# Performance work log

Hardware: AMD Instinct MI355X
Metric: run time of the kernel (lower is better)

Reference implementation:

```python
import jax, jax.numpy as jnp
import numpy as np

NQ = 4  # n_qubits_per_head


def _apply_ry(state, theta, q):
    # state: (N, 2,2,2,2) real amplitudes; theta: (N,) per-element angle; wire q
    st = jnp.moveaxis(state, 1 + q, -1)
    c = jnp.cos(0.5 * theta).reshape(-1, 1, 1, 1)
    s = jnp.sin(0.5 * theta).reshape(-1, 1, 1, 1)
    a0, a1 = st[..., 0], st[..., 1]
    st = jnp.stack([c * a0 - s * a1, s * a0 + c * a1], axis=-1)
    return jnp.moveaxis(st, -1, 1 + q)


def _apply_cnot(state, ctrl, tgt):
    st = jnp.moveaxis(state, (1 + ctrl, 1 + tgt), (-2, -1))
    st = jnp.stack([st[..., 0, :], st[..., 1, ::-1]], axis=-2)
    return jnp.moveaxis(st, (-2, -1), (1 + ctrl, 1 + tgt))


def _quantum_circuit(x_in, par):
    # x_in: (N, NQ) data angles; par: (N, L, NQ) variational angles (per head, tiled)
    N = x_in.shape[0]
    L = par.shape[1]
    state = jnp.zeros((N, 2, 2, 2, 2), x_in.dtype).at[:, 0, 0, 0, 0].set(1.0)
    for l in range(L):
        for q in range(NQ):
            state = _apply_ry(state, par[:, l, q], q)
        for q in range(NQ - 1):
            state = _apply_cnot(state, q, q + 1)
        state = _apply_cnot(state, NQ - 1, 0)
    for q in range(NQ):
        state = _apply_ry(state, x_in[:, q], q)
    p = state * state  # probabilities (real amplitudes: only RY/CNOT gates)
    zs = []
    for q in range(NQ):
        st = jnp.moveaxis(p, 1 + q, -1)
        zs.append(jnp.sum(st[..., 0], axis=(1, 2, 3)) - jnp.sum(st[..., 1], axis=(1, 2, 3)))
    return jnp.stack(zs, axis=-1)  # (N, NQ)


def setup_inputs() -> dict:
    key = jax.random.key(0)
    ks = jax.random.split(key, 6)
    B, T, E, H, L = 4, 2048, 1024, 16, 2
    scale = 1.0 / np.sqrt(E)
    x = jax.random.normal(ks[0], (B, T, E), dtype=jnp.float32)
    Wq = jax.random.normal(ks[1], (E, E), dtype=jnp.float32) * scale
    Wk = jax.random.normal(ks[2], (E, E), dtype=jnp.float32) * scale
    Wv = jax.random.normal(ks[3], (E, E), dtype=jnp.float32) * scale
    Wo = jax.random.normal(ks[4], (E, E), dtype=jnp.float32) * scale
    qparams = jax.random.normal(ks[5], (H, L, NQ), dtype=jnp.float32)
    return {"x": x, "Wq": Wq, "Wk": Wk, "Wv": Wv, "Wo": Wo, "qparams": qparams}


def reference(x, Wq, Wk, Wv, Wo, qparams):
    B, T, E = x.shape
    H, L, _ = qparams.shape
    hd = E // H
    q = x @ Wq.T
    k = x @ Wk.T
    v = x @ Wv.T
    # NOTE: original scales by sqrt(embed_dim), not sqrt(head_dim)
    scores = jnp.einsum('bte,bse->bts', q, k) / jnp.sqrt(jnp.asarray(E, x.dtype))
    w = jax.nn.softmax(scores, axis=-1)
    out = jnp.einsum('bts,bse->bte', w, v)
    oh = out.reshape(B, T, H, hd)
    N = B * T * H
    xin = oh[..., :NQ].reshape(N, NQ)
    par = jnp.broadcast_to(qparams[None, None], (B, T, H, L, NQ)).reshape(N, L, NQ)
    z = _quantum_circuit(xin, par)  # (N, NQ)
    zfull = jnp.concatenate([z, jnp.zeros((N, hd - NQ), x.dtype)], axis=-1)
    return zfull.reshape(B, T, E) @ Wo.T
```

## Files before the change

### kernel.cpp

```cpp
#include <hip/hip_runtime.h>
#include <hip/hip_fp16.h>

typedef _Float16 half_t;
typedef __attribute__((ext_vector_type(8))) _Float16 half8;
typedef __attribute__((ext_vector_type(4))) float floatx4;

__device__ __forceinline__ void async_copy16(const void* src, void* dst_lds) {
  __builtin_amdgcn_global_load_lds(
      (__attribute__((address_space(1))) void*)src,
      (__attribute__((address_space(3))) void*)dst_lds, 16, 0, 0);
}

__global__ __launch_bounds__(512, 2) void gemm_nt_256(
    const half_t* __restrict__ A, const half_t* __restrict__ B,
    half_t* __restrict__ C,
    int lda, int ldb, int ldc, int kIters,
    long sAz2, long sBz2, long sCz2, float scale)
{
  __shared__ __align__(16) half_t sm[2][2][256 * 64];

  const int tid  = threadIdx.x;
  const int wave = tid >> 6, lane = tid & 63;
  const int wm = wave >> 2, wn = wave & 3;
  const int er = lane >> 4, ec = lane & 15;
  const int sw = ec & 7;

  const long z = blockIdx.z;
  const half_t* Ab = A + (long)blockIdx.x * 256 * lda + z * sAz2;
  const half_t* Bb = B + (long)blockIdx.y * 256 * ldb + z * sBz2;

  const int srow = tid >> 3;
  const int skq  = (tid & 7) ^ (srow & 7);

  floatx4 acc[2][2][4][2];
  #pragma unroll
  for (int a = 0; a < 2; a++)
    #pragma unroll
    for (int b = 0; b < 2; b++)
      #pragma unroll
      for (int i = 0; i < 4; i++)
        #pragma unroll
        for (int j = 0; j < 2; j++)
          acc[a][b][i][j] = (floatx4){0.f, 0.f, 0.f, 0.f};

#define STAGE_A(bb, hf, kt) do {                                              \
    const half_t* Ak_ = Ab + (long)(kt) * 64;                                 \
    _Pragma("unroll")                                                         \
    for (int r_ = 0; r_ < 2; r_++) {                                          \
      int lrow_ = r_ * 64 + srow;                                             \
      async_copy16(Ak_ + (long)((hf) * 128 + lrow_) * lda + skq * 8,          \
                   &sm[(bb)][0][(hf) * 8192 + (r_ * 512 + wave * 64) * 8]);   \
    } } while (0)

#define STAGE_B(bb, hf, kt) do {                                              \
    const half_t* Bk_ = Bb + (long)(kt) * 64;                                 \
    _Pragma("unroll")                                                         \
    for (int r_ = 0; r_ < 2; r_++) {                                          \
      int lrow_ = r_ * 64 + srow;                                             \
      async_copy16(Bk_ + (long)((hf) * 128 + lrow_) * ldb + skq * 8,          \
                   &sm[(bb)][1][(hf) * 8192 + (r_ * 512 + wave * 64) * 8]);   \
    } } while (0)

#define DS_A(DST, BB, MH, KS) do {                                            \
    _Pragma("unroll")                                                         \
    for (int ii = 0; ii < 4; ii++) {                                          \
      int row_ = (MH) * 128 + wm * 64 + ii * 16 + ec;                         \
      DST[ii] = *(const half8*)                                               \
          &sm[BB][0][row_ * 64 + ((((KS) * 4 + er) ^ sw) * 8)];               \
    } } while (0)

#define DS_B(DST, BB, KS) do {                                                \
    _Pragma("unroll")                                                         \
    for (int nj = 0; nj < 4; nj++) {                                          \
      int row_ = (nj >> 1) * 128 + wn * 32 + (nj & 1) * 16 + ec;              \
      DST[nj] = *(const half8*)                                               \
          &sm[BB][1][row_ * 64 + ((((KS) * 4 + er) ^ sw) * 8)];               \
    } } while (0)

#define MFMA16(AF, BF, MH) do {                                               \
    __builtin_amdgcn_s_setprio(1);                                            \
    _Pragma("unroll")                                                         \
    for (int ii = 0; ii < 4; ii++)                                            \
      _Pragma("unroll")                                                       \
      for (int nj = 0; nj < 4; nj++)                                          \
        acc[MH][nj >> 1][ii][nj & 1] =                                        \
            __builtin_amdgcn_mfma_f32_16x16x32_f16(                           \
                AF[ii], BF[nj], acc[MH][nj >> 1][ii][nj & 1], 0, 0, 0);       \
    __builtin_amdgcn_s_setprio(0);                                            \
  } while (0)

#define BAR() __builtin_amdgcn_s_barrier()
#define VMW(N) asm volatile("s_waitcnt vmcnt(" #N ")" ::: "memory")

  half8 afA[4], afB[4], bfA[4], bfB[4];
  int cur = 0;
  const int nt = kIters;

  STAGE_B(0, 0, 0); STAGE_B(0, 1, 0); STAGE_A(0, 0, 0); STAGE_A(0, 1, 0);
  VMW(2);
  BAR();
  DS_A(afA, 0, 0, 0);
  DS_B(bfA, 0, 0);

  for (int n = 0; n < nt; ++n) {
    const int hasNext = (n + 1 < nt);
    DS_A(afB, cur, 0, 1);
    DS_B(bfB, cur, 1);
    if (hasNext) { STAGE_B(cur ^ 1, 0, n + 1); STAGE_B(cur ^ 1, 1, n + 1); }
    MFMA16(afA, bfA, 0);
    if (hasNext) { VMW(4); } else { VMW(0); }
    BAR();
    DS_A(afA, cur, 1, 0);
    if (hasNext) STAGE_A(cur ^ 1, 0, n + 1);
    MFMA16(afB, bfB, 0);
    BAR();
    DS_A(afB, cur, 1, 1);
    if (hasNext) STAGE_A(cur ^ 1, 1, n + 1);
    MFMA16(afA, bfA, 1);
    if (hasNext) VMW(2);
    BAR();
    if (hasNext) {
      DS_A(afA, cur ^ 1, 0, 0);
      DS_B(bfA, cur ^ 1, 0);
    }
    MFMA16(afB, bfB, 1);
    BAR();
    cur ^= 1;
  }

#undef STAGE_A
#undef STAGE_B
#undef DS_A
#undef DS_B
#undef MFMA16
#undef BAR
#undef VMW

  const long rowBase = (long)blockIdx.x * 256;
  const long colBase = (long)blockIdx.y * 256;
  half_t* Cz = C + z * sCz2;
  #pragma unroll
  for (int mh = 0; mh < 2; mh++)
    #pragma unroll
    for (int nh = 0; nh < 2; nh++)
      #pragma unroll
      for (int ii = 0; ii < 4; ii++)
        #pragma unroll
        for (int jj = 0; jj < 2; jj++)
          #pragma unroll
          for (int r = 0; r < 4; r++) {
            long row = rowBase + mh * 128 + wm * 64 + ii * 16 + er * 4 + r;
            long col = colBase + nh * 128 + wn * 32 + jj * 16 + ec;
            Cz[row * (long)ldc + col] =
                (_Float16)(acc[mh][nh][ii][jj][r] * scale);
          }
}

template<int BN, int EPI>
__global__ __launch_bounds__(256) void gemm_nt(
    const half_t* __restrict__ A, const half_t* __restrict__ B,
    void* __restrict__ Cout,
    int lda, int ldb, int ldc, int kIters, int zShift,
    long sAz1, long sBz1, long sCz1,
    long sAz2, long sBz2, long sCz2, float scale,
    const float* __restrict__ qab)
{
  constexpr int BM = 128;
  constexpr int WN = BN / 2;
  constexpr int AN = WN / 16;
  constexpr int RA = BM * 8 / 256;
  constexpr int RB = BN * 8 / 256;
  __shared__ __align__(16) half_t lA[BM * 64];
  __shared__ __align__(16) half_t lB[BN * 64];

  const int tid  = threadIdx.x;
  const int wave = tid >> 6, lane = tid & 63;
  const int wm = wave >> 1, wn = wave & 1;
  const int er = lane >> 4, ec = lane & 15;
  const int sw = ec & 7;

  const long z = blockIdx.z;
  const long z2 = z >> zShift;
  const long z1 = z - (z2 << zShift);
  const half_t* Ab = A + (long)blockIdx.x * BM * lda + z1 * sAz1 + z2 * sAz2;
  const half_t* Bb = B + (long)blockIdx.y * BN * ldb + z1 * sBz1 + z2 * sBz2;
  const long cz = z1 * sCz1 + z2 * sCz2;

  floatx4 acc[4][AN];
  #pragma unroll
  for (int i = 0; i < 4; i++)
    #pragma unroll
    for (int j = 0; j < AN; j++)
      acc[i][j] = (floatx4){0.f, 0.f, 0.f, 0.f};

  for (int ks = 0; ks < kIters; ++ks) {
    const half_t* Ak = Ab + ks * 64;
    const half_t* Bk = Bb + ks * 64;
    #pragma unroll
    for (int r = 0; r < RA; r++) {
      int s = r * 256 + tid;
      int row = s >> 3;
      int kq = (s & 7) ^ (row & 7);
      async_copy16(Ak + (long)row * lda + kq * 8,
                   &lA[(r * 256 + wave * 64) * 8]);
    }
    #pragma unroll
    for (int r = 0; r < RB; r++) {
      int s = r * 256 + tid;
      int row = s >> 3;
      int kq = (s & 7) ^ (row & 7);
      async_copy16(Bk + (long)row * ldb + kq * 8,
                   &lB[(r * 256 + wave * 64) * 8]);
    }
    __syncthreads();

    #pragma unroll
    for (int h = 0; h < 2; h++) {
      half8 af[4], bfv[AN];
      #pragma unroll
      for (int i = 0; i < 4; i++) {
        int row = wm * 64 + i * 16 + ec;
        af[i] = *(const half8*)&lA[row * 64 + (((h * 4 + er) ^ sw) * 8)];
      }
      #pragma unroll
      for (int j = 0; j < AN; j++) {
        int row = wn * WN + j * 16 + ec;
        bfv[j] = *(const half8*)&lB[row * 64 + (((h * 4 + er) ^ sw) * 8)];
      }
      #pragma unroll
      for (int i = 0; i < 4; i++)
        #pragma unroll
        for (int j = 0; j < AN; j++)
          acc[i][j] = __builtin_amdgcn_mfma_f32_16x16x32_f16(
              af[i], bfv[j], acc[i][j], 0, 0, 0);
    }
    __syncthreads();
  }

  const long rowBase = (long)blockIdx.x * BM + wm * 64;
  const long colBase = (long)blockIdx.y * BN + wn * WN;
  #pragma unroll
  for (int i = 0; i < 4; i++)
    #pragma unroll
    for (int j = 0; j < AN; j++)
      #pragma unroll
      for (int r = 0; r < 4; r++) {
        long row = rowBase + i * 16 + er * 4 + r;
        long col = colBase + j * 16 + ec;
        float v = acc[i][j][r];
        if constexpr (EPI == 0) {
          ((half_t*)Cout)[cz + row * (long)ldc + col] = (_Float16)(v * scale);
        } else if constexpr (EPI == 1) {
          ((half_t*)Cout)[cz + col * (long)ldc + row] = (_Float16)v;
        } else if constexpr (EPI == 2) {
          ((float*)Cout)[cz + row * (long)ldc + col] = v * scale;
        } else {
          float za = qab[2 * (int)col], zb = qab[2 * (int)col + 1];
          float zv = za * cosf(v) + zb * sinf(v);
          ((half_t*)Cout)[cz + row * (long)ldc + col] = (_Float16)zv;
        }
      }
}

__global__ __launch_bounds__(256) void softmax_rows(half_t* __restrict__ S,
                                                    int ld)
{
  const long row = blockIdx.x;
  half8* sp = (half8*)(S + row * (long)ld);
  const int t = threadIdx.x;
  const int wave = t >> 6, lane = t & 63;
  half8 hv = sp[t];
  float e[8];
  #pragma unroll
  for (int k = 0; k < 8; k++) e[k] = (float)hv[k];
  float m = e[0];
  #pragma unroll
  for (int k = 1; k < 8; k++) m = fmaxf(m, e[k]);
  #pragma unroll
  for (int o = 32; o > 0; o >>= 1) m = fmaxf(m, __shfl_xor(m, o));
  __shared__ float rmax[4], rsum[4];
  if (lane == 0) rmax[wave] = m;
  __syncthreads();
  m = fmaxf(fmaxf(rmax[0], rmax[1]), fmaxf(rmax[2], rmax[3]));
  float s = 0.f;
  #pragma unroll
  for (int k = 0; k < 8; k++) { e[k] = expf(e[k] - m); s += e[k]; }
  #pragma unroll
  for (int o = 32; o > 0; o >>= 1) s += __shfl_xor(s, o);
  if (lane == 0) rsum[wave] = s;
  __syncthreads();
  float inv = 1.f / (rsum[0] + rsum[1] + rsum[2] + rsum[3]);
  half8 o8;
  #pragma unroll
  for (int k = 0; k < 8; k++) o8[k] = (_Float16)(e[k] * inv);
  sp[t] = o8;
}

__global__ __launch_bounds__(256) void prep_all(
    const float* __restrict__ x,  const float* __restrict__ Wq,
    const float* __restrict__ Wk, const float* __restrict__ Wv,
    const float* __restrict__ Wo, const float* __restrict__ qp, int L,
    half_t* __restrict__ xh, half_t* __restrict__ Wqk,
    half_t* __restrict__ Wv4, half_t* __restrict__ Wos,
    float* __restrict__ qab)
{
  const int bid = blockIdx.x;
  if (bid < 4096) {
    long i = ((long)bid * 256 + threadIdx.x) * 8;
    float4 a = *(const float4*)(x + i);
    float4 b = *(const float4*)(x + i + 4);
    half8 h = {(_Float16)a.x, (_Float16)a.y, (_Float16)a.z, (_Float16)a.w,
               (_Float16)b.x, (_Float16)b.y, (_Float16)b.z, (_Float16)b.w};
    *(half8*)(xh + i) = h;
  } else if (bid < 5120) {
    long i = ((long)(bid - 4096) * 256 + threadIdx.x) * 8;
    int r = (int)(i >> 10);
    int e = (int)(i & 1023);
    const float* src = (r < 1024 ? Wq + (long)r * 1024
                                 : Wk + (long)(r - 1024) * 1024) + e;
    float4 a = *(const float4*)src;
    float4 b = *(const float4*)(src + 4);
    half8 h = {(_Float16)a.x, (_Float16)a.y, (_Float16)a.z, (_Float16)a.w,
               (_Float16)b.x, (_Float16)b.y, (_Float16)b.z, (_Float16)b.w};
    *(half8*)(Wqk + i) = h;
  } else if (bid < 5152) {
    long i = ((long)(bid - 5120) * 256 + threadIdx.x) * 8;
    int c = (int)(i >> 10);
    int e = (int)(i & 1023);
    const float* src = Wv + (long)(((c >> 2) << 6) | (c & 3)) * 1024 + e;
    float4 a = *(const float4*)src;
    float4 b = *(const float4*)(src + 4);
    half8 h = {(_Float16)a.x, (_Float16)a.y, (_Float16)a.z, (_Float16)a.w,
               (_Float16)b.x, (_Float16)b.y, (_Float16)b.z, (_Float16)b.w};
    *(half8*)(Wv4 + i) = h;
  } else if (bid < 5408) {
    int idx = (bid - 5152) * 256 + threadIdx.x;
    int e = idx >> 6, c = idx & 63;
    Wos[idx] = (_Float16)Wo[(long)e * 1024 + (((c >> 2) << 6) | (c & 3))];
  } else {
    int h = threadIdx.x;
    if (h >= 16) return;
    float st[16];
    #pragma unroll
    for (int i = 0; i < 16; i++) st[i] = 0.f;
    st[0] = 1.f;
    for (int l = 0; l < L; l++) {
      #pragma unroll
      for (int q = 0; q < 4; q++) {
        float th = qp[(h * L + l) * 4 + q];
        float c = cosf(0.5f * th), s = sinf(0.5f * th);
        int mq = 8 >> q;
        #pragma unroll
        for (int i = 0; i < 16; i++) {
          if ((i & mq) == 0) {
            float a0 = st[i], a1 = st[i | mq];
            st[i]      = c * a0 - s * a1;
            st[i | mq] = s * a0 + c * a1;
          }
        }
      }
      const int cm[4] = {8, 4, 2, 1};
      const int tm[4] = {4, 2, 1, 8};
      #pragma unroll
      for (int p = 0; p < 4; p++) {
        int mc = cm[p], mt = tm[p];
        #pragma unroll
        for (int i = 0; i < 16; i++) {
          if ((i & mc) != 0 && (i & mt) == 0) {
            float tv = st[i]; st[i] = st[i | mt]; st[i | mt] = tv;
          }
        }
      }
    }
    #pragma unroll
    for (int q = 0; q < 4; q++) {
      int mq = 8 >> q;
      float zc = 0.f, xc = 0.f;
      #pragma unroll
      for (int i = 0; i < 16; i++) {
        float p2 = st[i] * st[i];
        zc += ((i & mq) == 0) ? p2 : -p2;
        if ((i & mq) == 0) xc += st[i] * st[i | mq];
      }
      qab[(h * 4 + q) * 2 + 0] = zc;
      qab[(h * 4 + q) * 2 + 1] = -2.f * xc;
    }
  }
}

extern "C" void kernel_launch(void* const* d_in, const int* in_sizes, int n_in,
                              void* d_out, int out_size, void* d_ws, size_t ws_size,
                              hipStream_t stream)
{
  const float* x  = (const float*)d_in[0];
  const float* Wq = (const float*)d_in[1];
  const float* Wk = (const float*)d_in[2];
  const float* Wv = (const float*)d_in[3];
  const float* Wo = (const float*)d_in[4];
  const float* qp = (const float*)d_in[5];
  const int L = in_sizes[5] / 64;
  float* out = (float*)d_out;

  char* w = (char*)d_ws;
  size_t off = 0;
  auto alloc = [&](size_t bytes) -> void* {
    void* p = w + off;
    off = (off + bytes + 255) & ~(size_t)255;
    return p;
  };
  float*  qab  = (float*)alloc(512);
  half_t* xh   = (half_t*)alloc((size_t)8192 * 1024 * 2);
  half_t* Wqk  = (half_t*)alloc((size_t)2048 * 1024 * 2);
  half_t* Wv4  = (half_t*)alloc((size_t)64 * 1024 * 2);
  half_t* Wos  = (half_t*)alloc((size_t)1024 * 64 * 2);
  half_t* V4th = (half_t*)alloc((size_t)64 * 8192 * 2);
  half_t* Z4   = (half_t*)alloc((size_t)8192 * 64 * 2);

  half_t* QKb = (half_t*)d_out;

  int tier = (ws_size >= off + (size_t)8192 * 2048 * 2 + 256) ? 0 : 1;
  const size_t Sn = (tier == 0) ? (size_t)8192 * 2048 : (size_t)2048 * 2048;
  half_t* S = (half_t*)alloc(Sn * 2);

  prep_all<<<dim3(5409), dim3(256), 0, stream>>>(
      x, Wq, Wk, Wv, Wo, qp, L, xh, Wqk, Wv4, Wos, qab);

  gemm_nt_256<<<dim3(32, 8, 1), 512, 0, stream>>>(
      xh, Wqk, QKb, 1024, 1024, 2048, 16, 0, 0, 0, 1.f);
  gemm_nt<64, 1><<<dim3(64, 1, 1), 256, 0, stream>>>(
      xh, Wv4, V4th, 1024, 1024, 8192, 16, 0,
      0, 0, 0, 0, 0, 0, 1.f, nullptr);

  if (tier == 0) {
    gemm_nt_256<<<dim3(8, 8, 4), 512, 0, stream>>>(
        QKb, QKb + 1024, S, 2048, 2048, 2048, 16,
        (long)2048 * 2048, (long)2048 * 2048, (long)2048 * 2048, 0.03125f);
    softmax_rows<<<dim3(8192), dim3(256), 0, stream>>>(S, 2048);
    gemm_nt<64, 5><<<dim3(16, 1, 4), 256, 0, stream>>>(
        S, V4th, Z4, 2048, 8192, 64, 32, 0,
        0, 0, 0, (long)2048 * 2048, 2048, (long)2048 * 64, 1.f, qab);
  } else {
    for (int b = 0; b < 4; b++) {
      const long q0 = (long)b * 2048;
      gemm_nt<128, 0><<<dim3(16, 16, 1), 256, 0, stream>>>(
          QKb + q0 * 2048, QKb + 1024 + q0 * 2048, S,
          2048, 2048, 2048, 16, 0, 0, 0, 0, 0, 0, 0, 0.03125f, nullptr);
      softmax_rows<<<dim3(2048), dim3(256), 0, stream>>>(S, 2048);
      gemm_nt<64, 5><<<dim3(16, 1, 1), 256, 0, stream>>>(
          S, V4th + q0, Z4 + q0 * 64, 2048, 8192, 64, 32, 0,
          0, 0, 0, 0, 0, 0, 1.f, qab);
    }
  }

  gemm_nt<128, 2><<<dim3(64, 8, 1), 256, 0, stream>>>(
      Z4, Wos, out, 64, 64, 1024, 1, 0,
      0, 0, 0, 0, 0, 0, 1.f, nullptr);
}
```

Before: 239.7 us.

## Split-K the V and PV skinny GEMMs with separate reduction kernels

The skinny V4 projection GEMM (64 blocks) and the attention-times-V GEMM (64 blocks) each underfill the GPU. They are now split along K into 4 fp32 partial outputs, giving 256 blocks per launch, and small reduction kernels sum the partials. The quantum epilogue moves into the Z reduction kernel. This adds extra fp32 traffic through scratch buffers (S and d_out are reused as partial storage) and two more launches.

```diff
diff --git a/kernel.cpp b/kernel.cpp
--- a/kernel.cpp
+++ b/kernel.cpp
@@ -2,6 +2,7 @@
 #include <hip/hip_fp16.h>
 
 typedef _Float16 half_t;
+typedef __attribute__((ext_vector_type(4))) _Float16 half4;
 typedef __attribute__((ext_vector_type(8))) _Float16 half8;
 typedef __attribute__((ext_vector_type(4))) float floatx4;
 
@@ -254,12 +255,53 @@
           ((half_t*)Cout)[cz + col * (long)ldc + row] = (_Float16)v;
         } else if constexpr (EPI == 2) {
           ((float*)Cout)[cz + row * (long)ldc + col] = v * scale;
+        } else if constexpr (EPI == 4) {
+          ((float*)Cout)[cz + col * (long)ldc + row] = v;
         } else {
           float za = qab[2 * (int)col], zb = qab[2 * (int)col + 1];
           float zv = za * cosf(v) + zb * sinf(v);
           ((half_t*)Cout)[cz + row * (long)ldc + col] = (_Float16)zv;
         }
       }
+}
+
+__global__ __launch_bounds__(256) void v4_reduce(const float* __restrict__ P,
+                                                 half_t* __restrict__ O)
+{
+  const long CH = (long)64 * 8192;
+  long i = ((long)blockIdx.x * 256 + threadIdx.x) * 4;
+  float4 a = *(const float4*)(P + i);
+  float4 b = *(const float4*)(P + i + CH);
+  float4 c = *(const float4*)(P + i + 2 * CH);
+  float4 d = *(const float4*)(P + i + 3 * CH);
+  half4 o;
+  o[0] = (_Float16)(a.x + b.x + c.x + d.x);
+  o[1] = (_Float16)(a.y + b.y + c.y + d.y);
+  o[2] = (_Float16)(a.z + b.z + c.z + d.z);
+  o[3] = (_Float16)(a.w + b.w + c.w + d.w);
+  *(half4*)(O + i) = o;
+}
+
+__global__ __launch_bounds__(256) void z_reduce_quantum(
+    const float* __restrict__ P, const float* __restrict__ qab,
+    half_t* __restrict__ O)
+{
+  const long CH = (long)8192 * 64;
+  long i = ((long)blockIdx.x * 256 + threadIdx.x) * 4;
+  float4 a = *(const float4*)(P + i);
+  float4 b = *(const float4*)(P + i + CH);
+  float4 c = *(const float4*)(P + i + 2 * CH);
+  float4 d = *(const float4*)(P + i + 3 * CH);
+  float s[4] = {a.x + b.x + c.x + d.x, a.y + b.y + c.y + d.y,
+                a.z + b.z + c.z + d.z, a.w + b.w + c.w + d.w};
+  int c0 = (int)(i & 63);
+  half4 o;
+  #pragma unroll
+  for (int j = 0; j < 4; j++) {
+    float za = qab[2 * (c0 + j)], zb = qab[2 * (c0 + j) + 1];
+    o[j] = (_Float16)(za * cosf(s[j]) + zb * sinf(s[j]));
+  }
+  *(half4*)(O + i) = o;
 }
 
 __global__ __launch_bounds__(256) void softmax_rows(half_t* __restrict__ S,
@@ -427,19 +469,29 @@
 
   gemm_nt_256<<<dim3(32, 8, 1), 512, 0, stream>>>(
       xh, Wqk, QKb, 1024, 1024, 2048, 16, 0, 0, 0, 1.f);
-  gemm_nt<64, 1><<<dim3(64, 1, 1), 256, 0, stream>>>(
-      xh, Wv4, V4th, 1024, 1024, 8192, 16, 0,
-      0, 0, 0, 0, 0, 0, 1.f, nullptr);
 
   if (tier == 0) {
+    float* V4p = (float*)S;
+    gemm_nt<64, 4><<<dim3(64, 1, 4), 256, 0, stream>>>(
+        xh, Wv4, V4p, 1024, 1024, 8192, 4, 0,
+        0, 0, 0, 256, 256, (long)64 * 8192, 1.f, nullptr);
+    v4_reduce<<<dim3(512), dim3(256), 0, stream>>>(V4p, V4th);
+
     gemm_nt_256<<<dim3(8, 8, 4), 512, 0, stream>>>(
         QKb, QKb + 1024, S, 2048, 2048, 2048, 16,
         (long)2048 * 2048, (long)2048 * 2048, (long)2048 * 2048, 0.03125f);
     softmax_rows<<<dim3(8192), dim3(256), 0, stream>>>(S, 2048);
-    gemm_nt<64, 5><<<dim3(16, 1, 4), 256, 0, stream>>>(
-        S, V4th, Z4, 2048, 8192, 64, 32, 0,
-        0, 0, 0, (long)2048 * 2048, 2048, (long)2048 * 64, 1.f, qab);
+
+    float* Zp = (float*)d_out;
+    gemm_nt<64, 2><<<dim3(16, 1, 16), 256, 0, stream>>>(
+        S, V4th, Zp, 2048, 8192, 64, 8, 2,
+        (long)2048 * 2048, 2048, (long)2048 * 64,
+        512, 512, (long)8192 * 64, 1.f, nullptr);
+    z_reduce_quantum<<<dim3(512), dim3(256), 0, stream>>>(Zp, qab, Z4);
   } else {
+    gemm_nt<64, 1><<<dim3(64, 1, 1), 256, 0, stream>>>(
+        xh, Wv4, V4th, 1024, 1024, 8192, 16, 0,
+        0, 0, 0, 0, 0, 0, 1.f, nullptr);
     for (int b = 0; b < 4; b++) {
       const long q0 = (long)b * 2048;
       gemm_nt<128, 0><<<dim3(16, 16, 1), 256, 0, stream>>>(
```

Result: faster. 219.2 us (-8.5%).
